# Kernel optimization log

Hardware: AMD Instinct MI355X
Metric: run time of the kernel (lower is better)

## Reference

```python
import jax, jax.numpy as jnp
import numpy as np

MIN_DISP = -128
MAX_DISP = 0

N, C, H, W = 1, 16, 128, 256


def setup_inputs() -> dict:
    key = jax.random.key(0)
    k1, k2 = jax.random.split(key)
    left = jax.random.normal(k1, (N, C, H, W), dtype=jnp.float32)
    right = jax.random.normal(k2, (N, C, H, W), dtype=jnp.float32)
    return {"left": left, "right": right}


def reference(left, right):
    # Disparities i = MIN_DISP .. MAX_DISP-1 (all negative here).
    # For i < 0 (shift s = -i > 0) the torch code computes
    #   pad_bottom(left[:, :, :H-s, :] - right[:, :, s:, :], s)
    # i.e. out[n, d, c, h, w] = left[n,c,h,w] - right[n,c,h+s,w] if h+s < H else 0.
    n, c, h_dim, w_dim = left.shape
    disps = jnp.arange(MIN_DISP, MAX_DISP)          # [D]
    shifts = -disps                                  # [D], positive shifts
    s_max = int(-MIN_DISP)

    # Pad right along H so shifted reads are in-bounds (zeros past the edge).
    right_pad = jnp.pad(right, ((0, 0), (0, 0), (0, s_max), (0, 0)))
    idx = jnp.arange(h_dim)[None, :] + shifts[:, None]   # [D, H]
    right_shift = right_pad[:, :, idx, :]                # [N, C, D, H, W]

    mask = (idx < h_dim).astype(left.dtype)              # [D, H]
    cost = mask[None, None, :, :, None] * (left[:, :, None, :, :] - right_shift)
    # torch.stack(dim=1) -> [N, D, C, H, W]
    return jnp.transpose(cost, (0, 2, 1, 3, 4))
```

## Files before the change

### kernel.cpp

```cpp
#include <hip/hip_runtime.h>


typedef float f32x4 __attribute__((ext_vector_type(4)));

__global__ __launch_bounds__(256) void CostDifference_kernel(
    const f32x4* __restrict__ left,
    const f32x4* __restrict__ right,
    f32x4* __restrict__ out)
{
    const int lane = threadIdx.x & 63;

    const int x  = blockIdx.x & 7;
    const int k  = blockIdx.x >> 3;
    const int wk = (k << 2) | (threadIdx.x >> 6);
    const int second = (wk >= 264) ? 1 : 0;
    const int c     = (x << 1) | second;
    const int local = wk - second * 264;

    if (local < 120) {
        int p = local;
        int i = 0;
        while (p >= 15 - i) { p -= 15 - i; ++i; }
        const int j = i + 1 + p;

        const int i8 = i << 3, j8 = j << 3;
        f32x4 L[8], R[8];
#pragma unroll
        for (int a = 0; a < 8; ++a) L[a] = left [(c * 128 + i8 + a) * 64 + lane];
#pragma unroll
        for (int b = 0; b < 8; ++b) R[b] = right[(c * 128 + j8 + b) * 64 + lane];

        const int base = (128 + i8 - j8) * 2048 + c * 128 + i8;
#pragma unroll
        for (int ab = -7; ab <= 7; ++ab) {
            const int lo = ab > 0 ? ab : 0;
            const int hi = ab < 0 ? 7 + ab : 7;
#pragma unroll
            for (int a = lo; a <= hi; ++a) {
                const int b = a - ab;
                const int row = base + a + ab * 2048;
                f32x4 o;
                o.x = L[a].x - R[b].x;
                o.y = L[a].y - R[b].y;
                o.z = L[a].z - R[b].z;
                o.w = L[a].w - R[b].w;
                out[row * 64 + lane] = o;
            }
        }
    } else if (local < 136) {
        const int i8 = (local - 120) << 3;
        f32x4 L[8], R[8];
#pragma unroll
        for (int a = 0; a < 8; ++a) L[a] = left [(c * 128 + i8 + a) * 64 + lane];
#pragma unroll
        for (int b = 0; b < 8; ++b) R[b] = right[(c * 128 + i8 + b) * 64 + lane];

        const int base = 128 * 2048 + c * 128 + i8;
#pragma unroll
        for (int ab = -7; ab <= -1; ++ab) {
#pragma unroll
            for (int a = 0; a <= 7 + ab; ++a) {
                const int b = a - ab;
                const int row = base + a + ab * 2048;
                f32x4 o;
                o.x = L[a].x - R[b].x;
                o.y = L[a].y - R[b].y;
                o.z = L[a].z - R[b].z;
                o.w = L[a].w - R[b].w;
                out[row * 64 + lane] = o;
            }
        }
    } else {
        const int t    = local - 136;
        const int d    = t >> 1;
        const int half = t & 1;
        const int d2   = 127 - d;
        const int n1   = 128 - d;
        const int start = half ? 65 : 0;
        const int end   = half ? 129 : 65;
        const f32x4 zero = {0.f, 0.f, 0.f, 0.f};

        const int e1 = min(end, n1);
        int rb = (d * 2048 + c * 128 + d + start) * 64 + lane;
        for (int kk = start; kk < e1; ++kk, rb += 64) out[rb] = zero;

        const int s2 = max(start, n1);
        rb = (d2 * 2048 + c * 128 + d2 + (s2 - n1)) * 64 + lane;
        for (int kk = s2; kk < end; ++kk, rb += 64) out[rb] = zero;
    }
}

extern "C" void kernel_launch(void* const* d_in, const int* in_sizes, int n_in,
                              void* d_out, int out_size, void* d_ws, size_t ws_size,
                              hipStream_t stream) {
    const f32x4* left  = (const f32x4*)d_in[0];
    const f32x4* right = (const f32x4*)d_in[1];
    f32x4* out = (f32x4*)d_out;

    CostDifference_kernel<<<1056, 256, 0, stream>>>(left, right, out);
}
```

Before: 45.14 us.

## Share 16x16 row-block tiles through LDS across four waves per block

Off-diagonal work is regrouped into 16-row by 16-row block pairs per workgroup. The L and R rows are loaded once into shared memory and split into four 8x8 sub-tiles, one per wave, so each wave no longer reads its own rows from global memory. Diagonal-adjacent pairs, diagonal tiles and zero-fill work are remapped onto the remaining blocks per channel. Global input traffic drops, but the kernel now needs a barrier and LDS staging, and the cost is dominated by output writes anyway.

```diff
diff --git a/kernel.cpp b/kernel.cpp
--- a/kernel.cpp
+++ b/kernel.cpp
@@ -2,91 +2,116 @@
 
 
 typedef float f32x4 __attribute__((ext_vector_type(4)));
+
+__device__ __forceinline__ void store_tile(f32x4* __restrict__ out,
+                                           const f32x4 (&L)[8],
+                                           const f32x4 (&R)[8],
+                                           int base) {
+#pragma unroll
+    for (int ab = -7; ab <= 7; ++ab) {
+        const int lo = ab > 0 ? ab : 0;
+        const int hi = ab < 0 ? 7 + ab : 7;
+#pragma unroll
+        for (int a = lo; a <= hi; ++a) {
+            const int b = a - ab;
+            f32x4 o;
+            o.x = L[a].x - R[b].x;
+            o.y = L[a].y - R[b].y;
+            o.z = L[a].z - R[b].z;
+            o.w = L[a].w - R[b].w;
+            out[(base + a + ab * 2048) * 64] = o;
+        }
+    }
+}
 
 __global__ __launch_bounds__(256) void CostDifference_kernel(
     const f32x4* __restrict__ left,
     const f32x4* __restrict__ right,
     f32x4* __restrict__ out)
 {
+    __shared__ f32x4 lds[32][64];
     const int lane = threadIdx.x & 63;
+    const int w    = threadIdx.x >> 6;
 
-    const int x  = blockIdx.x & 7;
-    const int k  = blockIdx.x >> 3;
-    const int wk = (k << 2) | (threadIdx.x >> 6);
-    const int second = (wk >= 264) ? 1 : 0;
-    const int c     = (x << 1) | second;
-    const int local = wk - second * 264;
+    const int c = blockIdx.x / 66;
+    const int r = blockIdx.x - c * 66;
 
-    if (local < 120) {
-        int p = local;
-        int i = 0;
-        while (p >= 15 - i) { p -= 15 - i; ++i; }
-        const int j = i + 1 + p;
+    if (r < 28) {
+        int p = r, I = 0;
+        while (p >= 7 - I) { p -= 7 - I; ++I; }
+        const int J = I + 1 + p;
 
-        const int i8 = i << 3, j8 = j << 3;
+        const int base_l = (c * 128 + (I << 4)) * 64 + lane;
+        const int base_r = (c * 128 + (J << 4)) * 64 + lane;
+#pragma unroll
+        for (int k = 0; k < 8; ++k) {
+            const int row = (k << 2) + w;
+            lds[row][lane] = (row < 16) ? left [base_l + (row << 6)]
+                                        : right[base_r + ((row - 16) << 6)];
+        }
+        __syncthreads();
+
+        const int qa = (w >> 1) & 1, qb = w & 1;
         f32x4 L[8], R[8];
 #pragma unroll
-        for (int a = 0; a < 8; ++a) L[a] = left [(c * 128 + i8 + a) * 64 + lane];
+        for (int a = 0; a < 8; ++a) L[a] = lds[(qa << 3) + a][lane];
 #pragma unroll
-        for (int b = 0; b < 8; ++b) R[b] = right[(c * 128 + j8 + b) * 64 + lane];
+        for (int b = 0; b < 8; ++b) R[b] = lds[16 + (qb << 3) + b][lane];
 
+        const int i8 = (I << 4) + (qa << 3);
+        const int j8 = (J << 4) + (qb << 3);
         const int base = (128 + i8 - j8) * 2048 + c * 128 + i8;
+        store_tile(out + lane, L, R, base);
+    } else {
+        const int wk = ((r - 28) << 2) | w;
+        if (wk < 8) {
+            const int i8 = wk << 4, j8 = i8 + 8;
+            f32x4 L[8], R[8];
 #pragma unroll
-        for (int ab = -7; ab <= 7; ++ab) {
-            const int lo = ab > 0 ? ab : 0;
-            const int hi = ab < 0 ? 7 + ab : 7;
+            for (int a = 0; a < 8; ++a) L[a] = left [(c * 128 + i8 + a) * 64 + lane];
 #pragma unroll
-            for (int a = lo; a <= hi; ++a) {
-                const int b = a - ab;
-                const int row = base + a + ab * 2048;
-                f32x4 o;
-                o.x = L[a].x - R[b].x;
-                o.y = L[a].y - R[b].y;
-                o.z = L[a].z - R[b].z;
-                o.w = L[a].w - R[b].w;
-                out[row * 64 + lane] = o;
+            for (int b = 0; b < 8; ++b) R[b] = right[(c * 128 + j8 + b) * 64 + lane];
+            const int base = (128 + i8 - j8) * 2048 + c * 128 + i8;
+            store_tile(out + lane, L, R, base);
+        } else if (wk < 24) {
+            const int i8 = (wk - 8) << 3;
+            f32x4 L[8], R[8];
+#pragma unroll
+            for (int a = 0; a < 8; ++a) L[a] = left [(c * 128 + i8 + a) * 64 + lane];
+#pragma unroll
+            for (int b = 0; b < 8; ++b) R[b] = right[(c * 128 + i8 + b) * 64 + lane];
+            const int base = 128 * 2048 + c * 128 + i8;
+#pragma unroll
+            for (int ab = -7; ab <= -1; ++ab) {
+#pragma unroll
+                for (int a = 0; a <= 7 + ab; ++a) {
+                    const int b = a - ab;
+                    f32x4 o;
+                    o.x = L[a].x - R[b].x;
+                    o.y = L[a].y - R[b].y;
+                    o.z = L[a].z - R[b].z;
+                    o.w = L[a].w - R[b].w;
+                    out[(base + a + ab * 2048) * 64 + lane] = o;
+                }
             }
+        } else {
+            const int t    = wk - 24;
+            const int d    = t >> 1;
+            const int half = t & 1;
+            const int d2   = 127 - d;
+            const int n1   = 128 - d;
+            const int start = half ? 65 : 0;
+            const int end   = half ? 129 : 65;
+            const f32x4 zero = {0.f, 0.f, 0.f, 0.f};
+
+            const int e1 = min(end, n1);
+            int rb = (d * 2048 + c * 128 + d + start) * 64 + lane;
+            for (int kk = start; kk < e1; ++kk, rb += 64) out[rb] = zero;
+
+            const int s2 = max(start, n1);
+            rb = (d2 * 2048 + c * 128 + d2 + (s2 - n1)) * 64 + lane;
+            for (int kk = s2; kk < end; ++kk, rb += 64) out[rb] = zero;
         }
-    } else if (local < 136) {
-        const int i8 = (local - 120) << 3;
-        f32x4 L[8], R[8];
-#pragma unroll
-        for (int a = 0; a < 8; ++a) L[a] = left [(c * 128 + i8 + a) * 64 + lane];
-#pragma unroll
-        for (int b = 0; b < 8; ++b) R[b] = right[(c * 128 + i8 + b) * 64 + lane];
-
-        const int base = 128 * 2048 + c * 128 + i8;
-#pragma unroll
-        for (int ab = -7; ab <= -1; ++ab) {
-#pragma unroll
-            for (int a = 0; a <= 7 + ab; ++a) {
-                const int b = a - ab;
-                const int row = base + a + ab * 2048;
-                f32x4 o;
-                o.x = L[a].x - R[b].x;
-                o.y = L[a].y - R[b].y;
-                o.z = L[a].z - R[b].z;
-                o.w = L[a].w - R[b].w;
-                out[row * 64 + lane] = o;
-            }
-        }
-    } else {
-        const int t    = local - 136;
-        const int d    = t >> 1;
-        const int half = t & 1;
-        const int d2   = 127 - d;
-        const int n1   = 128 - d;
-        const int start = half ? 65 : 0;
-        const int end   = half ? 129 : 65;
-        const f32x4 zero = {0.f, 0.f, 0.f, 0.f};
-
-        const int e1 = min(end, n1);
-        int rb = (d * 2048 + c * 128 + d + start) * 64 + lane;
-        for (int kk = start; kk < e1; ++kk, rb += 64) out[rb] = zero;
-
-        const int s2 = max(start, n1);
-        rb = (d2 * 2048 + c * 128 + d2 + (s2 - n1)) * 64 + lane;
-        for (int kk = s2; kk < end; ++kk, rb += 64) out[rb] = zero;
     }
 }
 
```

Measured after the change: 42.21 us. -6.5%, faster.
